# Kernel tuning notes

Measured on AMD Instinct MI355X. Metric: run time of the kernel, lower is better.

## Reference

```python
import jax, jax.numpy as jnp
import numpy as np

K = 12          # tagset size incl START/STOP
START = 10
STOP = 11
NEG = -10000.0
B, T, V, D, H = 64, 1024, 50000, 256, 512
Hh = H // 2


def setup_inputs() -> dict:
    key = jax.random.key(0)
    ks = jax.random.split(key, 20)
    sentence = jax.random.randint(ks[0], (B, T), 1, V)
    seq_lens = jax.random.randint(ks[1], (B,), T // 2, T + 1)
    emb = jax.random.normal(ks[2], (V, D), dtype=jnp.float32) * 0.1
    emb = emb.at[0].set(0.0)  # padding_idx=0
    s = 1.0 / np.sqrt(Hh)

    def u(k, shape):
        return jax.random.uniform(k, shape, minval=-s, maxval=s, dtype=jnp.float32)

    Wih_f = u(ks[3], (4 * Hh, D)); Whh_f = u(ks[4], (4 * Hh, Hh))
    bih_f = u(ks[5], (4 * Hh,));  bhh_f = u(ks[6], (4 * Hh,))
    Wih_b = u(ks[7], (4 * Hh, D)); Whh_b = u(ks[8], (4 * Hh, Hh))
    bih_b = u(ks[9], (4 * Hh,));  bhh_b = u(ks[10], (4 * Hh,))
    sl = 1.0 / np.sqrt(H)
    Wtag = jax.random.uniform(ks[11], (K, H), minval=-sl, maxval=sl, dtype=jnp.float32)
    btag = jax.random.uniform(ks[12], (K,), minval=-sl, maxval=sl, dtype=jnp.float32)
    transitions = jax.random.normal(ks[13], (K, K), dtype=jnp.float32)
    transitions = transitions.at[START, :].set(NEG).at[:, STOP].set(NEG)
    h0 = jax.random.normal(ks[14], (2, B, Hh), dtype=jnp.float32)
    c0 = jax.random.normal(ks[15], (2, B, Hh), dtype=jnp.float32)
    return dict(sentence=sentence, seq_lens=seq_lens, emb=emb,
                Wih_f=Wih_f, Whh_f=Whh_f, bih_f=bih_f, bhh_f=bhh_f,
                Wih_b=Wih_b, Whh_b=Whh_b, bih_b=bih_b, bhh_b=bhh_b,
                Wtag=Wtag, btag=btag, transitions=transitions, h0=h0, c0=c0)


def _lstm_dir(x, mask, h0, c0, Wih, Whh, bih, bhh, reverse):
    # x: [B,T,D], mask: [B,T] bool. Masked steps keep the carried state
    # (equivalent to PyTorch packed-sequence semantics for positions < seq_len).
    def step(carry, inp):
        h, c = carry
        xt, mt = inp  # [B,D], [B,1]
        z = xt @ Wih.T + h @ Whh.T + bih + bhh  # [B,4Hh], torch gate order i,f,g,o
        i, f, g, o = jnp.split(z, 4, axis=-1)
        c2 = jax.nn.sigmoid(f) * c + jax.nn.sigmoid(i) * jnp.tanh(g)
        h2 = jax.nn.sigmoid(o) * jnp.tanh(c2)
        h = jnp.where(mt, h2, h)
        c = jnp.where(mt, c2, c)
        return (h, c), h
    xs = (x.transpose(1, 0, 2), mask.T[:, :, None])
    _, hs = jax.lax.scan(step, (h0, c0), xs, reverse=reverse)
    return hs.transpose(1, 0, 2)  # [B,T,Hh]


def reference(sentence, seq_lens, emb, Wih_f, Whh_f, bih_f, bhh_f,
              Wih_b, Whh_b, bih_b, bhh_b, Wtag, btag, transitions, h0, c0):
    Bn, Tn = sentence.shape
    mask = jnp.arange(Tn)[None, :] < seq_lens[:, None]  # [B,T]
    x = emb[sentence]  # [B,T,D]
    hf = _lstm_dir(x, mask, h0[0], c0[0], Wih_f, Whh_f, bih_f, bhh_f, False)
    hb = _lstm_dir(x, mask, h0[1], c0[1], Wih_b, Whh_b, bih_b, bhh_b, True)
    feats = jnp.concatenate([hf, hb], -1) @ Wtag.T + btag  # [B,T,K]

    # Vectorized Viterbi over batch and tags (replaces per-tag python loops)
    fv0 = jnp.full((Bn, K), NEG, dtype=feats.dtype).at[:, START].set(0.0)
    ident = jnp.arange(K)[None, :]

    def vstep(fv, inp):
        ft, mt = inp  # [B,K], [B]
        sc = fv[:, None, :] + transitions[None, :, :]  # [B,Knext,Kprev]
        bp = jnp.argmax(sc, -1)                        # [B,K]
        vmax = jnp.max(sc, -1) + ft
        fv2 = jnp.where(mt[:, None], vmax, fv)
        bp = jnp.where(mt[:, None], bp, ident)         # identity passthrough on pad
        return fv2, bp

    fv, bptrs = jax.lax.scan(vstep, fv0, (feats.transpose(1, 0, 2), mask.T))
    term = fv + transitions[STOP][None, :]
    best = jnp.argmax(term, -1)   # [B]
    score = jnp.max(term, -1)     # [B]

    def btrace(tag, bp):
        prev = jnp.take_along_axis(bp, tag[:, None], 1)[:, 0]
        return prev, tag

    _, path = jax.lax.scan(btrace, best, bptrs, reverse=True)  # [T,B]
    path = jnp.where(mask, path.T, 0)  # [B,T], zeros beyond seq_len
    return score, path
```

## Files before the change

kernel.cpp:

```cpp
#include <hip/hip_runtime.h>
#include <math.h>

#define NEG10K -10000.0f

static const size_t OFF_WT_IH = 0;
static const size_t OFF_WT_HH = 524288;
static const size_t OFF_BIAS  = 1048576;
static const size_t OFF_WTAGD = 1050624;
static const size_t OFF_BTAG  = 1058816;
static const size_t OFF_FEATS = 1058832;
static const size_t OFF_HC    = 3155984;
static const size_t OFF_CC    = 3188752;
static const size_t OFF_PUB   = 3221520;
static const size_t OFF_G     = 3352592;

__device__ __forceinline__ float sigf(float x) { return 1.0f / (1.0f + expf(-x)); }

__global__ __launch_bounds__(256) void k_transpose(
    const float* __restrict__ wih_f, const float* __restrict__ wih_b,
    const float* __restrict__ whh_f, const float* __restrict__ whh_b,
    float* __restrict__ ws) {
  __shared__ float tile[32][33];
  int z = blockIdx.z;
  const float* src = (z == 0) ? wih_f : (z == 1) ? wih_b : (z == 2) ? whh_f : whh_b;
  float* dst = ws + ((z < 2) ? (OFF_WT_IH + (size_t)z * 262144)
                             : (OFF_WT_HH + (size_t)(z - 2) * 262144));
  int r0 = blockIdx.y * 32;
  int c0 = blockIdx.x * 32;
  int tid = threadIdx.x;
  int c = tid & 31, rg = tid >> 5;
#pragma unroll
  for (int i = 0; i < 4; ++i) {
    int r = rg * 4 + i;
    tile[r][c] = src[(size_t)(r0 + r) * 256 + c0 + c];
  }
  __syncthreads();
  int r2 = tid & 31, cg = tid >> 5;
#pragma unroll
  for (int i = 0; i < 4; ++i) {
    int ccv = cg * 4 + i;
    dst[(size_t)(c0 + ccv) * 1024 + r0 + r2] = tile[r2][ccv];
  }
}

__global__ __launch_bounds__(256) void k_prep_small(
    const float* __restrict__ bih_f, const float* __restrict__ bhh_f,
    const float* __restrict__ bih_b, const float* __restrict__ bhh_b,
    const float* __restrict__ wtag, const float* __restrict__ btag,
    float* __restrict__ ws) {
  int i = blockIdx.x * 256 + threadIdx.x;
  if (i < 2048) {
    int d = i >> 10, n = i & 1023;
    ws[OFF_BIAS + i] = d ? (bih_b[n] + bhh_b[n]) : (bih_f[n] + bhh_f[n]);
  } else if (i < 2048 + 8192) {
    int r = i - 2048;
    int d = r >> 12, rem = r & 4095;
    int k = rem >> 8, j = rem & 255;
    ws[OFF_WTAGD + r] = (k < 12) ? wtag[(size_t)k * 512 + d * 256 + j] : 0.0f;
  } else if (i < 2048 + 8192 + 16) {
    int kk = i - 10240;
    ws[OFF_BTAG + kk] = (kk < 12) ? btag[kk] : 0.0f;
  } else if (i < 10256 + 131072) {
    ws[OFF_PUB + (i - 10256)] = 0.0f;
  }
}

__global__ __launch_bounds__(256) void k_gemm_g(
    const int* __restrict__ sentence, const float* __restrict__ emb,
    const float* __restrict__ ws_c, float* __restrict__ G,
    int t0, int cshift) {
  __shared__ float As[32][64];
  __shared__ float Bs[32][64];
  __shared__ int idx_s[64];
  int d = blockIdx.z;
  int m0 = blockIdx.y * 64, n0 = blockIdx.x * 64;
  int tid = threadIdx.x;
  int cmask = (1 << cshift) - 1;
  const float* Wt = ws_c + OFF_WT_IH + (size_t)d * 262144;
  if (tid < 64) {
    int m = m0 + tid;
    int b = m >> cshift, tt = m & cmask;
    int t = d ? (1023 - t0 - tt) : (t0 + tt);
    idx_s[tid] = sentence[(size_t)b * 1024 + t];
  }
  __syncthreads();
  float acc[4][4] = {};
  int tm = tid >> 4, tn = tid & 15;
  int am = tid & 63, ak = (tid >> 6) * 8;
  int bn = (tid & 15) * 4, bk = tid >> 4;
  for (int k0 = 0; k0 < 256; k0 += 32) {
    const float* ar = emb + (size_t)idx_s[am] * 256 + k0 + ak;
    float4 a0 = *(const float4*)ar;
    float4 a1 = *(const float4*)(ar + 4);
    float4 b0 = *(const float4*)(Wt + (size_t)(k0 + bk) * 1024 + n0 + bn);
    float4 b1 = *(const float4*)(Wt + (size_t)(k0 + bk + 16) * 1024 + n0 + bn);
    As[ak + 0][am] = a0.x; As[ak + 1][am] = a0.y; As[ak + 2][am] = a0.z; As[ak + 3][am] = a0.w;
    As[ak + 4][am] = a1.x; As[ak + 5][am] = a1.y; As[ak + 6][am] = a1.z; As[ak + 7][am] = a1.w;
    *(float4*)&Bs[bk][bn] = b0;
    *(float4*)&Bs[bk + 16][bn] = b1;
    __syncthreads();
#pragma unroll
    for (int kk = 0; kk < 32; ++kk) {
      float4 av = *(const float4*)&As[kk][tm * 4];
      float4 bv = *(const float4*)&Bs[kk][tn * 4];
      float avf[4] = {av.x, av.y, av.z, av.w};
      float bvf[4] = {bv.x, bv.y, bv.z, bv.w};
#pragma unroll
      for (int i = 0; i < 4; ++i)
#pragma unroll
        for (int j = 0; j < 4; ++j) acc[i][j] = fmaf(avf[i], bvf[j], acc[i][j]);
    }
    __syncthreads();
  }
  float4 bias = *(const float4*)(ws_c + OFF_BIAS + (size_t)d * 1024 + n0 + tn * 4);
#pragma unroll
  for (int i = 0; i < 4; ++i) {
    int m = m0 + tm * 4 + i;
    int b = m >> cshift, tt = m & cmask;
    float* gp = G + (((size_t)d * 64 + b) * (size_t)(cmask + 1) + tt) * 1024 + n0 + tn * 4;
    float4 v;
    v.x = acc[i][0] + bias.x; v.y = acc[i][1] + bias.y;
    v.z = acc[i][2] + bias.z; v.w = acc[i][3] + bias.w;
    *(float4*)gp = v;
  }
}

#define FMA4(A, W, S) { A.x = fmaf(W.x, S, A.x); A.y = fmaf(W.y, S, A.y); \
                        A.z = fmaf(W.z, S, A.z); A.w = fmaf(W.w, S, A.w); }
__global__ __launch_bounds__(512) void k_lstm_split(
    const float* __restrict__ ws_c, const float* __restrict__ G,
    const float* __restrict__ h0p, const float* __restrict__ c0p,
    const int* __restrict__ seq_lens, float* __restrict__ ws_mut,
    int t0, int chunkT, int first) {
  __shared__ float zpart[8][4][128];
  __shared__ float zs[4][128];
  __shared__ float h_s[4][256];
  __shared__ float ldspad[16384];

  int bx = blockIdx.x;
  int w   = (bx >> 3) & 7;
  int gid = (bx & 7) + ((bx >> 6) << 3);
  int d   = gid >> 4;
  int bq4 = (gid & 15) * 4;
  int u0  = w * 32;
  int tid = threadIdx.x;
  if (first == 777) {
    ldspad[tid] = (float)tid; __syncthreads(); zs[0][0] = ldspad[tid ^ 1];
  }

  int cg = tid & 31, kq = tid >> 5;
  int c4 = cg * 4;
  int wv = tid >> 6, ln = tid & 63;

  const float* WhhT = ws_c + OFF_WT_HH + (size_t)d * 262144;
  int wcol = (cg >> 3) * 256 + u0 + (cg & 7) * 4;
  float4 wr[16];
#pragma unroll
  for (int i = 0; i < 16; ++i)
    wr[i] = *(const float4*)(WhhT + (size_t)(kq * 16 + i) * 1024 + wcol);

  const float* hsrc = first ? h0p : (ws_c + OFF_HC);
  for (int i = tid; i < 1024; i += 512) {
    int b = i >> 8, u = i & 255;
    h_s[b][u] = hsrc[((size_t)d * 64 + bq4 + b) * 256 + u];
  }
  float cc = 0.0f; int mylen = 0;
  int ob = tid >> 5, ou = tid & 31;
  if (tid < 128) {
    const float* csrc = first ? c0p : (ws_c + OFF_CC);
    cc = csrc[((size_t)d * 64 + bq4 + ob) * 256 + u0 + ou];
    mylen = seq_lens[bq4 + ob];
  }
  int tb_b = wv >> 1;
  int tb_k = (wv & 1) * 8 + (ln >> 3);
  int tb_j = ln & 7;
  float wtag_r[32];
  {
    const float* wtg = ws_c + OFF_WTAGD + (size_t)d * 4096 + tb_k * 256;
#pragma unroll
    for (int i = 0; i < 32; ++i) wtag_r[i] = wtg[tb_j + 8 * i];
  }
  unsigned long long* pub64 = (unsigned long long*)(ws_mut + OFF_PUB);
  float* featsD = ws_mut + OFF_FEATS + (size_t)d * 1048576;
  int bB = tid >> 7, jB = tid & 127;
  int gb = tid >> 8, gu = tid & 255;
  bool bail = false;
  __syncthreads();

  for (int s = 0; s < chunkT; ++s) {
    int gs = t0 + s;
    int t = d ? (1023 - gs) : gs;
    int p = gs & 1;
    unsigned tag = (unsigned)(gs + 1);
    float gval = G[(((size_t)d * 64 + bq4 + bB) * (size_t)chunkT + s) * 1024 +
                   (jB >> 5) * 256 + u0 + (jB & 31)];
    float4 acc[4] = {{0,0,0,0},{0,0,0,0},{0,0,0,0},{0,0,0,0}};
#pragma unroll
    for (int i = 0; i < 4; ++i) {
      int k = kq * 16 + i * 4;
      float4 w0 = wr[i * 4], w1 = wr[i * 4 + 1], w2 = wr[i * 4 + 2], w3 = wr[i * 4 + 3];
#pragma unroll
      for (int b = 0; b < 4; ++b) {
        float4 hv = *(const float4*)&h_s[b][k];
        FMA4(acc[b], w0, hv.x); FMA4(acc[b], w1, hv.y);
        FMA4(acc[b], w2, hv.z); FMA4(acc[b], w3, hv.w);
      }
    }
#pragma unroll
    for (int b = 0; b < 4; ++b) {
      acc[b].x += __shfl_xor(acc[b].x, 32);
      acc[b].y += __shfl_xor(acc[b].y, 32);
      acc[b].z += __shfl_xor(acc[b].z, 32);
      acc[b].w += __shfl_xor(acc[b].w, 32);
    }
    if ((tid & 32) == 0) {
#pragma unroll
      for (int b = 0; b < 4; ++b) *(float4*)&zpart[wv][b][c4] = acc[b];
    }
    __syncthreads();
    zs[bB][jB] = zpart[0][bB][jB] + zpart[1][bB][jB] + zpart[2][bB][jB] + zpart[3][bB][jB] +
                 zpart[4][bB][jB] + zpart[5][bB][jB] + zpart[6][bB][jB] + zpart[7][bB][jB] + gval;
    __syncthreads();
    if (tid < 128) {
      float zi = zs[ob][ou], zf = zs[ob][32 + ou], zg = zs[ob][64 + ou], zo = zs[ob][96 + ou];
      float cn = sigf(zf) * cc + sigf(zi) * tanhf(zg);
      float hn = sigf(zo) * tanhf(cn);
      bool m = t < mylen;
      cc = m ? cn : cc;
      float hp = m ? hn : h_s[ob][u0 + ou];
      union { float f; unsigned u; } hb; hb.f = hp;
      unsigned long long pk = ((unsigned long long)tag << 32) | (unsigned long long)hb.u;
      __hip_atomic_store(
          pub64 + (size_t)p * 32768 + ((size_t)d * 64 + bq4 + ob) * 256 + (u0 + ou),
          pk, __ATOMIC_RELAXED, __HIP_MEMORY_SCOPE_AGENT);
    }
    if (s > 0) {
      int tp = d ? (1023 - (gs - 1)) : (gs - 1);
      float pv = 0.0f;
#pragma unroll
      for (int i = 0; i < 32; ++i)
        pv = fmaf(h_s[tb_b][tb_j + 8 * i], wtag_r[i], pv);
      pv += __shfl_xor(pv, 1);
      pv += __shfl_xor(pv, 2);
      pv += __shfl_xor(pv, 4);
      if (w == 0 && tb_j == 0)
        featsD[(size_t)(bq4 + tb_b) * 16384 + (size_t)tp * 16 + tb_k] = pv;
    }
    __syncthreads();
    {
      size_t base = (size_t)p * 32768 + ((size_t)d * 64 + bq4) * 256;
      size_t i0 = base + (size_t)gb * 256 + gu;
      size_t i1 = i0 + 512;
      unsigned long long v0 =
          __hip_atomic_load(pub64 + i0, __ATOMIC_RELAXED, __HIP_MEMORY_SCOPE_AGENT);
      unsigned long long v1 =
          __hip_atomic_load(pub64 + i1, __ATOMIC_RELAXED, __HIP_MEMORY_SCOPE_AGENT);
      unsigned spin = 0;
      while ((((unsigned)(v0 >> 32) != tag) || ((unsigned)(v1 >> 32) != tag)) && !bail) {
        __builtin_amdgcn_s_sleep(1);
        if ((unsigned)(v0 >> 32) != tag)
          v0 = __hip_atomic_load(pub64 + i0, __ATOMIC_RELAXED, __HIP_MEMORY_SCOPE_AGENT);
        if ((unsigned)(v1 >> 32) != tag)
          v1 = __hip_atomic_load(pub64 + i1, __ATOMIC_RELAXED, __HIP_MEMORY_SCOPE_AGENT);
        if (++spin > 2000000u) { bail = true; break; }
      }
      union { unsigned u32; float f; } cv0, cv1;
      cv0.u32 = (unsigned)v0; cv1.u32 = (unsigned)v1;
      h_s[gb][gu]     = cv0.f;
      h_s[gb + 2][gu] = cv1.f;
    }
    __syncthreads();
  }
  {
    int tl = d ? (1023 - (t0 + chunkT - 1)) : (t0 + chunkT - 1);
    float pv = 0.0f;
#pragma unroll
    for (int i = 0; i < 32; ++i)
      pv = fmaf(h_s[tb_b][tb_j + 8 * i], wtag_r[i], pv);
    pv += __shfl_xor(pv, 1);
    pv += __shfl_xor(pv, 2);
    pv += __shfl_xor(pv, 4);
    if (w == 0 && tb_j == 0)
      featsD[(size_t)(bq4 + tb_b) * 16384 + (size_t)tl * 16 + tb_k] = pv;
  }
  if (tid < 128)
    ws_mut[OFF_CC + ((size_t)d * 64 + bq4 + ob) * 256 + u0 + ou] = cc;
  if (w == 0)
    for (int i = tid; i < 1024; i += 512)
      ws_mut[OFF_HC + ((size_t)d * 64 + bq4 + (i >> 8)) * 256 + (i & 255)] = h_s[i >> 8][i & 255];
}

__global__ __launch_bounds__(256) void k_lstm_fused(
    const float* __restrict__ ws_c, const int* __restrict__ sentence,
    const float* __restrict__ emb, const float* __restrict__ h0p,
    const float* __restrict__ c0p, const int* __restrict__ seq_lens,
    float* __restrict__ ws_mut) {
  int d = blockIdx.x & 1;
  int pr = blockIdx.x >> 1;
  int b0 = pr * 2, b1 = b0 + 1;
  const float* Wih = ws_c + OFF_WT_IH + (size_t)d * 262144;
  const float* Whh = ws_c + OFF_WT_HH + (size_t)d * 262144;
  __shared__ float h_s[2][256];
  __shared__ float x_s[2][2][256];
  __shared__ float z_s[2][1024];
  __shared__ int   sent_s[2][1024];
  __shared__ float wt_s[16][260];
  __shared__ float pfp_s[2][16][8];
  int tid = threadIdx.x;
  int len0 = seq_lens[b0], len1 = seq_lens[b1];
  for (int i = tid; i < 2048; i += 256)
    sent_s[i >> 10][i & 1023] = sentence[(size_t)(b0 + (i >> 10)) * 1024 + (i & 1023)];
  for (int i = tid; i < 4096; i += 256)
    wt_s[i >> 8][i & 255] = ws_c[OFF_WTAGD + (size_t)d * 4096 + i];
  h_s[0][tid] = h0p[((size_t)d * 64 + b0) * 256 + tid];
  h_s[1][tid] = h0p[((size_t)d * 64 + b1) * 256 + tid];
  float cc0 = c0p[((size_t)d * 64 + b0) * 256 + tid];
  float cc1 = c0p[((size_t)d * 64 + b1) * 256 + tid];
  int c4 = tid * 4;
  float4 bias_v = *(const float4*)(ws_c + OFF_BIAS + (size_t)d * 1024 + c4);
  __syncthreads();
  int t0 = d ? 1023 : 0;
  if (tid < 128) {
    int bb = tid >> 6, l = tid & 63;
    int row = sent_s[bb][t0];
    *(float4*)&x_s[0][bb][l * 4] = *(const float4*)(emb + (size_t)row * 256 + l * 4);
  }
  __syncthreads();
  float* featsD = ws_mut + OFF_FEATS + (size_t)d * 1048576;
  for (int s = 0; s < 1024; ++s) {
    int t = d ? (1023 - s) : s;
    int cur = s & 1, nxt = cur ^ 1;
    float4 pf = {0, 0, 0, 0};
    if (tid < 128) {
      int sn = (s < 1023) ? (s + 1) : 1023;
      int tn = d ? (1023 - sn) : sn;
      int bb = tid >> 6, l = tid & 63;
      pf = *(const float4*)(emb + (size_t)sent_s[bb][tn] * 256 + l * 4);
    }
    float4 a0 = bias_v, a1 = bias_v;
#pragma unroll 4
    for (int k = 0; k < 256; k += 4) {
      float4 xv0 = *(const float4*)&x_s[cur][0][k];
      float4 xv1 = *(const float4*)&x_s[cur][1][k];
      float4 hv0 = *(const float4*)&h_s[0][k];
      float4 hv1 = *(const float4*)&h_s[1][k];
      const float* wi = Wih + (size_t)k * 1024 + c4;
      const float* wh = Whh + (size_t)k * 1024 + c4;
      float4 wi0 = *(const float4*)(wi);
      float4 wi1 = *(const float4*)(wi + 1024);
      float4 wi2 = *(const float4*)(wi + 2048);
      float4 wi3 = *(const float4*)(wi + 3072);
      float4 wh0 = *(const float4*)(wh);
      float4 wh1 = *(const float4*)(wh + 1024);
      float4 wh2 = *(const float4*)(wh + 2048);
      float4 wh3 = *(const float4*)(wh + 3072);
      FMA4(a0, wi0, xv0.x); FMA4(a0, wi1, xv0.y); FMA4(a0, wi2, xv0.z); FMA4(a0, wi3, xv0.w);
      FMA4(a0, wh0, hv0.x); FMA4(a0, wh1, hv0.y); FMA4(a0, wh2, hv0.z); FMA4(a0, wh3, hv0.w);
      FMA4(a1, wi0, xv1.x); FMA4(a1, wi1, xv1.y); FMA4(a1, wi2, xv1.z); FMA4(a1, wi3, xv1.w);
      FMA4(a1, wh0, hv1.x); FMA4(a1, wh1, hv1.y); FMA4(a1, wh2, hv1.z); FMA4(a1, wh3, hv1.w);
    }
    *(float4*)&z_s[0][c4] = a0;
    *(float4*)&z_s[1][c4] = a1;
    __syncthreads();
    {
      float iv = z_s[0][tid], fv = z_s[0][tid + 256];
      float gv = z_s[0][tid + 512], ov = z_s[0][tid + 768];
      float cn = sigf(fv) * cc0 + sigf(iv) * tanhf(gv);
      float hn = sigf(ov) * tanhf(cn);
      bool m = t < len0;
      cc0 = m ? cn : cc0;
      h_s[0][tid] = m ? hn : h_s[0][tid];
    }
    {
      float iv = z_s[1][tid], fv = z_s[1][tid + 256];
      float gv = z_s[1][tid + 512], ov = z_s[1][tid + 768];
      float cn = sigf(fv) * cc1 + sigf(iv) * tanhf(gv);
      float hn = sigf(ov) * tanhf(cn);
      bool m = t < len1;
      cc1 = m ? cn : cc1;
      h_s[1][tid] = m ? hn : h_s[1][tid];
    }
    if (tid < 128) {
      int bb = tid >> 6, l = tid & 63;
      *(float4*)&x_s[nxt][bb][l * 4] = pf;
    }
    __syncthreads();
    {
      int b2 = tid >> 7, r = tid & 127;
      int ks = r >> 3, jg = r & 7;
      const float* hv = &h_s[b2][jg * 32];
      const float* wv = &wt_s[ks][jg * 32];
      float p = 0.0f;
#pragma unroll
      for (int i = 0; i < 32; ++i) p = fmaf(hv[i], wv[i], p);
      pfp_s[b2][ks][jg] = p;
    }
    __syncthreads();
    if (tid < 32) {
      int b = tid >> 4, k = tid & 15;
      float sum = 0.0f;
#pragma unroll
      for (int i = 0; i < 8; ++i) sum += pfp_s[b][k][i];
      featsD[(size_t)(b0 + b) * 16384 + (size_t)t * 16 + k] = sum;
    }
  }
}

__global__ __launch_bounds__(64) void k_viterbi(const float* __restrict__ ws_c,
                                                const float* __restrict__ trans,
                                                const int* __restrict__ seq_lens,
                                                float* __restrict__ out) {
  __shared__ char bp_s[1024][12];
  int b = blockIdx.x, lane = threadIdx.x;
  int len = seq_lens[b];
  float trow[12];
#pragma unroll
  for (int p = 0; p < 12; ++p) trow[p] = (lane < 12) ? trans[lane * 12 + p] : 0.0f;
  float tb = (lane < 16) ? ws_c[OFF_BTAG + lane] : 0.0f;
  float fv = (lane == 10) ? 0.0f : NEG10K;
  const float* ff = ws_c + OFF_FEATS + (size_t)b * 16384;
  const float* fb = ws_c + OFF_FEATS + 1048576 + (size_t)b * 16384;
  for (int t = 0; t < 1024; ++t) {
    float ft = (lane < 16) ? (ff[t * 16 + lane] + fb[t * 16 + lane] + tb) : 0.0f;
    float best = -3.0e38f; int arg = 0;
#pragma unroll
    for (int p = 0; p < 12; ++p) {
      float s = __shfl(fv, p) + trow[p];
      if (s > best) { best = s; arg = p; }
    }
    bool m = t < len;
    if (m) fv = best + ft;
    if (lane < 12) bp_s[t][lane] = (char)(m ? arg : lane);
  }
  float term = (lane < 12) ? fv + trans[132 + lane] : -3.0e38f;
  float bestv = -3.0e38f; int bestp = 0;
#pragma unroll
  for (int p = 0; p < 12; ++p) {
    float v = __shfl(term, p);
    if (v > bestv) { bestv = v; bestp = p; }
  }
  __syncthreads();
  if (lane == 0) {
    out[b] = bestv;
    int tag = bestp;
    float* po = out + 64 + (size_t)b * 1024;
    for (int t = 1023; t >= 0; --t) {
      po[t] = (t < len) ? (float)tag : 0.0f;
      tag = bp_s[t][tag];
    }
  }
}

extern "C" void kernel_launch(void* const* d_in, const int* in_sizes, int n_in,
                              void* d_out, int out_size, void* d_ws, size_t ws_size,
                              hipStream_t stream) {
  (void)in_sizes; (void)n_in; (void)out_size;
  const int*   sentence = (const int*)d_in[0];
  const int*   seq_lens = (const int*)d_in[1];
  const float* emb      = (const float*)d_in[2];
  const float* wih_f    = (const float*)d_in[3];
  const float* whh_f    = (const float*)d_in[4];
  const float* bih_f    = (const float*)d_in[5];
  const float* bhh_f    = (const float*)d_in[6];
  const float* wih_b    = (const float*)d_in[7];
  const float* whh_b    = (const float*)d_in[8];
  const float* bih_b    = (const float*)d_in[9];
  const float* bhh_b    = (const float*)d_in[10];
  const float* wtag     = (const float*)d_in[11];
  const float* btag     = (const float*)d_in[12];
  const float* trans    = (const float*)d_in[13];
  const float* h0p      = (const float*)d_in[14];
  const float* c0p      = (const float*)d_in[15];
  float* ws  = (float*)d_ws;
  float* out = (float*)d_out;
  size_t avail = ws_size / 4;
  if (avail < OFF_FEATS + 2097152) return;

  int chunkT = 0;
  const int opts[5] = {512, 256, 128, 64, 32};
  for (int i = 0; i < 5; ++i)
    if (OFF_G + (size_t)131072 * opts[i] <= avail) { chunkT = opts[i]; break; }

  k_transpose<<<dim3(8, 32, 4), 256, 0, stream>>>(wih_f, wih_b, whh_f, whh_b, ws);
  k_prep_small<<<553, 256, 0, stream>>>(bih_f, bhh_f, bih_b, bhh_b, wtag, btag, ws);
  if (chunkT) {
    int cshift = 31 - __builtin_clz(chunkT);
    int nc = 1024 / chunkT;
    for (int c = 0; c < nc; ++c) {
      int t0 = c * chunkT;
      k_gemm_g<<<dim3(16, chunkT, 2), 256, 0, stream>>>(sentence, emb, ws, ws + OFF_G,
                                                        t0, cshift);
      k_lstm_split<<<256, 512, 0, stream>>>(ws, ws + OFF_G, h0p, c0p, seq_lens, ws,
                                            t0, chunkT, c == 0);
    }
  } else {
    k_lstm_fused<<<64, 256, 0, stream>>>(ws, sentence, emb, h0p, c0p, seq_lens, ws);
  }
  k_viterbi<<<64, 64, 0, stream>>>(ws, trans, seq_lens, out);
}
```

Baseline: 4.053 ms.

## Fuse input projection into persistent LSTM kernel and drop chunked G GEMM

Removes the separate chunked embedding×Wih GEMM and its large G buffer. The persistent LSTM kernel now keeps Wih columns in registers alongside Whh, prefetches the next token's embedding into double-buffered shared memory, and computes the next step's input contribution while spinning on the cross-block h exchange. This is meant to eliminate the G round-trip through global memory and the repeated kernel launches, and to hide the input matmul inside the synchronization wait. The cost is doubled register pressure for weights and extra per-step FMA work on the serial critical path.

```diff
diff --git a/kernel.cpp b/kernel.cpp
--- a/kernel.cpp
+++ b/kernel.cpp
@@ -12,7 +12,7 @@
 static const size_t OFF_HC    = 3155984;
 static const size_t OFF_CC    = 3188752;
 static const size_t OFF_PUB   = 3221520;
-static const size_t OFF_G     = 3352592;
+static const size_t OFF_END   = 3352592;
 
 __device__ __forceinline__ float sigf(float x) { return 1.0f / (1.0f + expf(-x)); }
 
@@ -65,77 +65,19 @@
   }
 }
 
-__global__ __launch_bounds__(256) void k_gemm_g(
-    const int* __restrict__ sentence, const float* __restrict__ emb,
-    const float* __restrict__ ws_c, float* __restrict__ G,
-    int t0, int cshift) {
-  __shared__ float As[32][64];
-  __shared__ float Bs[32][64];
-  __shared__ int idx_s[64];
-  int d = blockIdx.z;
-  int m0 = blockIdx.y * 64, n0 = blockIdx.x * 64;
-  int tid = threadIdx.x;
-  int cmask = (1 << cshift) - 1;
-  const float* Wt = ws_c + OFF_WT_IH + (size_t)d * 262144;
-  if (tid < 64) {
-    int m = m0 + tid;
-    int b = m >> cshift, tt = m & cmask;
-    int t = d ? (1023 - t0 - tt) : (t0 + tt);
-    idx_s[tid] = sentence[(size_t)b * 1024 + t];
-  }
-  __syncthreads();
-  float acc[4][4] = {};
-  int tm = tid >> 4, tn = tid & 15;
-  int am = tid & 63, ak = (tid >> 6) * 8;
-  int bn = (tid & 15) * 4, bk = tid >> 4;
-  for (int k0 = 0; k0 < 256; k0 += 32) {
-    const float* ar = emb + (size_t)idx_s[am] * 256 + k0 + ak;
-    float4 a0 = *(const float4*)ar;
-    float4 a1 = *(const float4*)(ar + 4);
-    float4 b0 = *(const float4*)(Wt + (size_t)(k0 + bk) * 1024 + n0 + bn);
-    float4 b1 = *(const float4*)(Wt + (size_t)(k0 + bk + 16) * 1024 + n0 + bn);
-    As[ak + 0][am] = a0.x; As[ak + 1][am] = a0.y; As[ak + 2][am] = a0.z; As[ak + 3][am] = a0.w;
-    As[ak + 4][am] = a1.x; As[ak + 5][am] = a1.y; As[ak + 6][am] = a1.z; As[ak + 7][am] = a1.w;
-    *(float4*)&Bs[bk][bn] = b0;
-    *(float4*)&Bs[bk + 16][bn] = b1;
-    __syncthreads();
-#pragma unroll
-    for (int kk = 0; kk < 32; ++kk) {
-      float4 av = *(const float4*)&As[kk][tm * 4];
-      float4 bv = *(const float4*)&Bs[kk][tn * 4];
-      float avf[4] = {av.x, av.y, av.z, av.w};
-      float bvf[4] = {bv.x, bv.y, bv.z, bv.w};
-#pragma unroll
-      for (int i = 0; i < 4; ++i)
-#pragma unroll
-        for (int j = 0; j < 4; ++j) acc[i][j] = fmaf(avf[i], bvf[j], acc[i][j]);
-    }
-    __syncthreads();
-  }
-  float4 bias = *(const float4*)(ws_c + OFF_BIAS + (size_t)d * 1024 + n0 + tn * 4);
-#pragma unroll
-  for (int i = 0; i < 4; ++i) {
-    int m = m0 + tm * 4 + i;
-    int b = m >> cshift, tt = m & cmask;
-    float* gp = G + (((size_t)d * 64 + b) * (size_t)(cmask + 1) + tt) * 1024 + n0 + tn * 4;
-    float4 v;
-    v.x = acc[i][0] + bias.x; v.y = acc[i][1] + bias.y;
-    v.z = acc[i][2] + bias.z; v.w = acc[i][3] + bias.w;
-    *(float4*)gp = v;
-  }
-}
-
 #define FMA4(A, W, S) { A.x = fmaf(W.x, S, A.x); A.y = fmaf(W.y, S, A.y); \
                         A.z = fmaf(W.z, S, A.z); A.w = fmaf(W.w, S, A.w); }
 __global__ __launch_bounds__(512) void k_lstm_split(
-    const float* __restrict__ ws_c, const float* __restrict__ G,
-    const float* __restrict__ h0p, const float* __restrict__ c0p,
-    const int* __restrict__ seq_lens, float* __restrict__ ws_mut,
-    int t0, int chunkT, int first) {
+    const float* __restrict__ ws_c, const int* __restrict__ sentence,
+    const float* __restrict__ emb, const float* __restrict__ h0p,
+    const float* __restrict__ c0p, const int* __restrict__ seq_lens,
+    float* __restrict__ ws_mut, int first) {
   __shared__ float zpart[8][4][128];
   __shared__ float zs[4][128];
   __shared__ float h_s[4][256];
-  __shared__ float ldspad[16384];
+  __shared__ float x_s[2][4][256];
+  __shared__ int   sent_s[4][1024];
+  __shared__ float ldspad[10240];
 
   int bx = blockIdx.x;
   int w   = (bx >> 3) & 7;
@@ -152,24 +94,38 @@
   int c4 = cg * 4;
   int wv = tid >> 6, ln = tid & 63;
 
+  for (int i = tid; i < 4096; i += 512)
+    sent_s[i >> 10][i & 1023] = sentence[(size_t)(bq4 + (i >> 10)) * 1024 + (i & 1023)];
+  __syncthreads();
+
   const float* WhhT = ws_c + OFF_WT_HH + (size_t)d * 262144;
+  const float* WihT = ws_c + OFF_WT_IH + (size_t)d * 262144;
   int wcol = (cg >> 3) * 256 + u0 + (cg & 7) * 4;
-  float4 wr[16];
-#pragma unroll
-  for (int i = 0; i < 16; ++i)
-    wr[i] = *(const float4*)(WhhT + (size_t)(kq * 16 + i) * 1024 + wcol);
-
-  const float* hsrc = first ? h0p : (ws_c + OFF_HC);
+  float4 wh[16], wi[16];
+#pragma unroll
+  for (int i = 0; i < 16; ++i) {
+    wh[i] = *(const float4*)(WhhT + (size_t)(kq * 16 + i) * 1024 + wcol);
+    wi[i] = *(const float4*)(WihT + (size_t)(kq * 16 + i) * 1024 + wcol);
+  }
+
   for (int i = tid; i < 1024; i += 512) {
     int b = i >> 8, u = i & 255;
-    h_s[b][u] = hsrc[((size_t)d * 64 + bq4 + b) * 256 + u];
+    h_s[b][u] = h0p[((size_t)d * 64 + bq4 + b) * 256 + u];
   }
   float cc = 0.0f; int mylen = 0;
   int ob = tid >> 5, ou = tid & 31;
   if (tid < 128) {
-    const float* csrc = first ? c0p : (ws_c + OFF_CC);
-    cc = csrc[((size_t)d * 64 + bq4 + ob) * 256 + u0 + ou];
+    cc = c0p[((size_t)d * 64 + bq4 + ob) * 256 + u0 + ou];
     mylen = seq_lens[bq4 + ob];
+  }
+  int bB = tid >> 7, jB = tid & 127;
+  int colB = ((jB >> 5) << 8) + u0 + (jB & 31);
+  float biasB = ws_c[OFF_BIAS + (size_t)d * 1024 + colB];
+  int xb = tid >> 7, xj = (tid & 127) * 2;
+  {
+    int tt = d ? 1023 : 0;
+    float2 v = *(const float2*)(emb + (size_t)sent_s[xb][tt] * 256 + xj);
+    x_s[0][xb][xj] = v.x; x_s[0][xb][xj + 1] = v.y;
   }
   int tb_b = wv >> 1;
   int tb_k = (wv & 1) * 8 + (ln >> 3);
@@ -182,23 +138,41 @@
   }
   unsigned long long* pub64 = (unsigned long long*)(ws_mut + OFF_PUB);
   float* featsD = ws_mut + OFF_FEATS + (size_t)d * 1048576;
-  int bB = tid >> 7, jB = tid & 127;
   int gb = tid >> 8, gu = tid & 255;
   bool bail = false;
   __syncthreads();
 
-  for (int s = 0; s < chunkT; ++s) {
-    int gs = t0 + s;
-    int t = d ? (1023 - gs) : gs;
-    int p = gs & 1;
-    unsigned tag = (unsigned)(gs + 1);
-    float gval = G[(((size_t)d * 64 + bq4 + bB) * (size_t)chunkT + s) * 1024 +
-                   (jB >> 5) * 256 + u0 + (jB & 31)];
-    float4 acc[4] = {{0,0,0,0},{0,0,0,0},{0,0,0,0},{0,0,0,0}};
+  float4 acc_carry[4] = {{0,0,0,0},{0,0,0,0},{0,0,0,0},{0,0,0,0}};
+#pragma unroll
+  for (int i = 0; i < 4; ++i) {
+    int k = kq * 16 + i * 4;
+    float4 q0 = wi[i * 4], q1 = wi[i * 4 + 1], q2 = wi[i * 4 + 2], q3 = wi[i * 4 + 3];
+#pragma unroll
+    for (int b = 0; b < 4; ++b) {
+      float4 xv = *(const float4*)&x_s[0][b][k];
+      FMA4(acc_carry[b], q0, xv.x); FMA4(acc_carry[b], q1, xv.y);
+      FMA4(acc_carry[b], q2, xv.z); FMA4(acc_carry[b], q3, xv.w);
+    }
+  }
+
+  for (int s = 0; s < 1024; ++s) {
+    int t = d ? (1023 - s) : s;
+    int p = s & 1;
+    int cur = s & 1, nxt = cur ^ 1;
+    unsigned tag = (unsigned)(s + 1);
+    float2 xpf;
+    {
+      int sn = (s + 1 < 1024) ? (s + 1) : s;
+      int tn = d ? (1023 - sn) : sn;
+      xpf = *(const float2*)(emb + (size_t)sent_s[xb][tn] * 256 + xj);
+    }
+    float4 acc[4];
+#pragma unroll
+    for (int b = 0; b < 4; ++b) acc[b] = acc_carry[b];
 #pragma unroll
     for (int i = 0; i < 4; ++i) {
       int k = kq * 16 + i * 4;
-      float4 w0 = wr[i * 4], w1 = wr[i * 4 + 1], w2 = wr[i * 4 + 2], w3 = wr[i * 4 + 3];
+      float4 w0 = wh[i * 4], w1 = wh[i * 4 + 1], w2 = wh[i * 4 + 2], w3 = wh[i * 4 + 3];
 #pragma unroll
       for (int b = 0; b < 4; ++b) {
         float4 hv = *(const float4*)&h_s[b][k];
@@ -219,7 +193,8 @@
     }
     __syncthreads();
     zs[bB][jB] = zpart[0][bB][jB] + zpart[1][bB][jB] + zpart[2][bB][jB] + zpart[3][bB][jB] +
-                 zpart[4][bB][jB] + zpart[5][bB][jB] + zpart[6][bB][jB] + zpart[7][bB][jB] + gval;
+                 zpart[4][bB][jB] + zpart[5][bB][jB] + zpart[6][bB][jB] + zpart[7][bB][jB] + biasB;
+    x_s[nxt][xb][xj] = xpf.x; x_s[nxt][xb][xj + 1] = xpf.y;
     __syncthreads();
     if (tid < 128) {
       float zi = zs[ob][ou], zf = zs[ob][32 + ou], zg = zs[ob][64 + ou], zo = zs[ob][96 + ou];
@@ -235,7 +210,7 @@
           pk, __ATOMIC_RELAXED, __HIP_MEMORY_SCOPE_AGENT);
     }
     if (s > 0) {
-      int tp = d ? (1023 - (gs - 1)) : (gs - 1);
+      int tp = d ? (1023 - (s - 1)) : (s - 1);
       float pv = 0.0f;
 #pragma unroll
       for (int i = 0; i < 32; ++i)
@@ -255,6 +230,22 @@
           __hip_atomic_load(pub64 + i0, __ATOMIC_RELAXED, __HIP_MEMORY_SCOPE_AGENT);
       unsigned long long v1 =
           __hip_atomic_load(pub64 + i1, __ATOMIC_RELAXED, __HIP_MEMORY_SCOPE_AGENT);
+      if (s + 1 < 1024) {
+#pragma unroll
+        for (int b = 0; b < 4; ++b) { acc_carry[b].x = 0; acc_carry[b].y = 0;
+                                      acc_carry[b].z = 0; acc_carry[b].w = 0; }
+#pragma unroll
+        for (int i = 0; i < 4; ++i) {
+          int k = kq * 16 + i * 4;
+          float4 q0 = wi[i * 4], q1 = wi[i * 4 + 1], q2 = wi[i * 4 + 2], q3 = wi[i * 4 + 3];
+#pragma unroll
+          for (int b = 0; b < 4; ++b) {
+            float4 xv = *(const float4*)&x_s[nxt][b][k];
+            FMA4(acc_carry[b], q0, xv.x); FMA4(acc_carry[b], q1, xv.y);
+            FMA4(acc_carry[b], q2, xv.z); FMA4(acc_carry[b], q3, xv.w);
+          }
+        }
+      }
       unsigned spin = 0;
       while ((((unsigned)(v0 >> 32) != tag) || ((unsigned)(v1 >> 32) != tag)) && !bail) {
         __builtin_amdgcn_s_sleep(1);
@@ -272,7 +263,6 @@
     __syncthreads();
   }
   {
-    int tl = d ? (1023 - (t0 + chunkT - 1)) : (t0 + chunkT - 1);
     float pv = 0.0f;
 #pragma unroll
     for (int i = 0; i < 32; ++i)
@@ -280,14 +270,10 @@
     pv += __shfl_xor(pv, 1);
     pv += __shfl_xor(pv, 2);
     pv += __shfl_xor(pv, 4);
+    int tl = d ? 0 : 1023;
     if (w == 0 && tb_j == 0)
       featsD[(size_t)(bq4 + tb_b) * 16384 + (size_t)tl * 16 + tb_k] = pv;
   }
-  if (tid < 128)
-    ws_mut[OFF_CC + ((size_t)d * 64 + bq4 + ob) * 256 + u0 + ou] = cc;
-  if (w == 0)
-    for (int i = tid; i < 1024; i += 512)
-      ws_mut[OFF_HC + ((size_t)d * 64 + bq4 + (i >> 8)) * 256 + (i & 255)] = h_s[i >> 8][i & 255];
 }
 
 __global__ __launch_bounds__(256) void k_lstm_fused(
@@ -476,23 +462,10 @@
   size_t avail = ws_size / 4;
   if (avail < OFF_FEATS + 2097152) return;
 
-  int chunkT = 0;
-  const int opts[5] = {512, 256, 128, 64, 32};
-  for (int i = 0; i < 5; ++i)
-    if (OFF_G + (size_t)131072 * opts[i] <= avail) { chunkT = opts[i]; break; }
-
   k_transpose<<<dim3(8, 32, 4), 256, 0, stream>>>(wih_f, wih_b, whh_f, whh_b, ws);
   k_prep_small<<<553, 256, 0, stream>>>(bih_f, bhh_f, bih_b, bhh_b, wtag, btag, ws);
-  if (chunkT) {
-    int cshift = 31 - __builtin_clz(chunkT);
-    int nc = 1024 / chunkT;
-    for (int c = 0; c < nc; ++c) {
-      int t0 = c * chunkT;
-      k_gemm_g<<<dim3(16, chunkT, 2), 256, 0, stream>>>(sentence, emb, ws, ws + OFF_G,
-                                                        t0, cshift);
-      k_lstm_split<<<256, 512, 0, stream>>>(ws, ws + OFF_G, h0p, c0p, seq_lens, ws,
-                                            t0, chunkT, c == 0);
-    }
+  if (avail >= OFF_END) {
+    k_lstm_split<<<256, 512, 0, stream>>>(ws, sentence, emb, h0p, c0p, seq_lens, ws, 1);
   } else {
     k_lstm_fused<<<64, 256, 0, stream>>>(ws, sentence, emb, h0p, c0p, seq_lens, ws);
   }
```

Result: faster. 3.651 ms (-9.9%).
